# Performance work log

Hardware: AMD Instinct MI355X
Metric: run time of the kernel (lower is better)

The kernel has to match this reference:

```python
import jax, jax.numpy as jnp
import numpy as np

B, D, H = 512, 1024, 2048          # batch, context_dim, l_hidden
MAX_STEPS = 8                       # config.max_l_steps
ATOL = 0.01                         # config.l_conv_atol
THR = 0.1                           # config.commitment_threshold


def setup_inputs() -> dict:
    key = jax.random.key(0)
    ks = jax.random.split(key, 20)
    mat = lambda k, shp, fi: jax.random.normal(k, shp, jnp.float32) / np.float32(np.sqrt(fi))
    inp = dict(
        enc=jax.random.normal(ks[0], (B, D), jnp.float32),
        static_context=jax.random.normal(ks[1], (B, D), jnp.float32),
        # fresh RWKV state: channel 3 (pp, running max-exponent) = -1e30
        l_state=jnp.zeros((B, H, 5), jnp.float32).at[:, :, 3].set(-1e30),
        initial_drift=0.1 * jax.random.normal(ks[2], (B, D), jnp.float32),
        # l_input_proj: Linear(2*D -> H)
        Win=mat(ks[3], (2 * D, H), 2 * D), b_in=jnp.zeros((H,), jnp.float32),
        # context_drift_proj: Linear(H -> D, bias=False)
        Wdrift=mat(ks[4], (H, D), H),
        # l_to_out: Linear(H -> D)
        Wout=mat(ks[5], (H, D), H), b_out=jnp.zeros((D,), jnp.float32),
        # RWKV cell (v4-style) parameters over hidden dim H
        mix_k=jax.random.uniform(ks[6], (H,), jnp.float32),
        mix_v=jax.random.uniform(ks[7], (H,), jnp.float32),
        mix_r=jax.random.uniform(ks[8], (H,), jnp.float32),
        mix_k2=jax.random.uniform(ks[9], (H,), jnp.float32),
        mix_r2=jax.random.uniform(ks[10], (H,), jnp.float32),
        time_decay=0.5 * jax.random.normal(ks[11], (H,), jnp.float32),
        time_first=0.5 * jax.random.normal(ks[12], (H,), jnp.float32),
        Wk=mat(ks[13], (H, H), H), Wv=mat(ks[14], (H, H), H),
        Wr=mat(ks[15], (H, H), H), Wo=mat(ks[16], (H, H), H),
        Wk2=mat(ks[17], (H, H), H), Wv2=mat(ks[18], (H, H), H),
        Wr2=mat(ks[19], (H, H), H),
    )
    return inp


def _forward(enc, static_context, l_state, initial_drift, Win, b_in, Wdrift, Wout, b_out,
             mix_k, mix_v, mix_r, mix_k2, mix_r2, time_decay, time_first,
             Wk, Wv, Wr, Wo, Wk2, Wv2, Wr2):
    def cell(x, state):
        # RWKV-style linear-attention cell. state: [B,H,5] = (x_prev_tm, aa, bb, pp, x_prev_cm)
        xx, aa, bb, pp, cc = (state[..., i] for i in range(5))
        xk = x * mix_k + xx * (1.0 - mix_k)
        xv = x * mix_v + xx * (1.0 - mix_v)
        xr = x * mix_r + xx * (1.0 - mix_r)
        r = jax.nn.sigmoid(xr @ Wr)
        k = xk @ Wk
        v = xv @ Wv
        ww = time_first + k
        q = jnp.maximum(pp, ww)
        e1 = jnp.exp(pp - q); e2 = jnp.exp(ww - q)
        wkv = (e1 * aa + e2 * v) / (e1 * bb + e2)
        ww2 = pp - jnp.exp(time_decay)
        q2 = jnp.maximum(ww2, k)
        e1b = jnp.exp(ww2 - q2); e2b = jnp.exp(k - q2)
        tm_out = (r * wkv) @ Wo
        # channel-mix half of the cell (state channel 4)
        xk2 = x * mix_k2 + cc * (1.0 - mix_k2)
        xr2 = x * mix_r2 + cc * (1.0 - mix_r2)
        r2 = jax.nn.sigmoid(xr2 @ Wr2)
        kk = jnp.square(jax.nn.relu(xk2 @ Wk2))
        out = tm_out + r2 * (kk @ Wv2)
        new_state = jnp.stack([x, e1b * aa + e2b * v, e1b * bb + e2b, q2, x], axis=-1)
        return out, new_state

    def l_input_of(drift):
        v = jnp.concatenate([enc, static_context + drift], axis=-1) @ Win + b_in
        return jnp.clip(v, -50.0, 50.0)

    def step(carry, _):
        drift, sstate, done, csum, cnt = carry
        li = l_input_of(drift)
        out, ns = cell(li, sstate)
        ns = jnp.clip(ns, -50.0, 50.0)
        delta = jnp.tanh(out @ Wdrift)
        nd = jnp.clip(drift + delta, -5.0, 5.0)
        hinge = jnp.minimum(jax.nn.relu(jnp.mean(jnp.sum(nd * nd, axis=-1)) - THR), 100.0)
        conv = jnp.mean(jnp.abs(delta)) < ATOL
        # freeze all updates once converged (early-exit semantics under jit)
        drift = jnp.where(done, drift, nd)
        sstate = jnp.where(done, sstate, ns)
        csum = jnp.where(done, csum, csum + hinge)
        cnt = jnp.where(done, cnt, cnt + 1.0)
        done = jnp.logical_or(done, conv)
        return (drift, sstate, done, csum, cnt), None

    carry0 = (initial_drift, l_state, jnp.array(False), jnp.float32(0.0), jnp.float32(0.0))
    (drift, _, _, csum, cnt), _ = jax.lax.scan(step, carry0, None, length=MAX_STEPS)

    # final commit step uses the ORIGINAL l_state (not the shadow state)
    li = l_input_of(drift)
    final_out, next_state = cell(li, l_state)
    next_state = jnp.clip(next_state, -50.0, 50.0)
    final_enc = enc + final_out @ Wout + b_out
    commitment = csum / jnp.maximum(cnt, 1.0)
    return final_enc, next_state, commitment, drift


def reference(enc, static_context, l_state, initial_drift, Win, b_in, Wdrift, Wout, b_out,
              mix_k, mix_v, mix_r, mix_k2, mix_r2, time_decay, time_first,
              Wk, Wv, Wr, Wo, Wk2, Wv2, Wr2):
    return _forward(enc, static_context, l_state, initial_drift, Win, b_in, Wdrift, Wout, b_out,
                    mix_k, mix_v, mix_r, mix_k2, mix_r2, time_decay, time_first,
                    Wk, Wv, Wr, Wo, Wk2, Wv2, Wr2)
```

## Files before the change

### kernel.cpp

```cpp
#include <hip/hip_runtime.h>
#include <hip/hip_bf16.h>

#define Bb 512
#define Dd 1024
#define Hh 2048
#define BH_ (Bb*Hh)
#define BD_ (Bb*Dd)

typedef unsigned short u16;
typedef __attribute__((ext_vector_type(8))) short short8;
typedef __attribute__((ext_vector_type(4))) float f32x4;

enum { M_F32 = 0, M_IN, M_SIG, M_SQRELU, M_MIX, M_BF16, M_DRIFT, M_FINAL };

struct GemmP {
    const u16* A[5];
    const u16* W[5];
    void* dst[5];
    int mode[5];
    int M, N, K;
    int dstride;
    const int* done;
    const float* bias;
    const float* mk; const float* mv; const float* mr; const float* mk2v; const float* mr2v;
    float* xx; float* cc;
    const float* lstate;
    float* liF;
    float* stateOut;
    u16 *o1, *o2, *o3, *o4, *o5;
    const float* Kp; const float* Vp; const float* Rp;
    float* aa; float* bbp; float* ppp;
    const float* Li;
    const float* tf; const float* td;
    const float* R2;
    u16* acat35;
    float* drift; float* accAbs; float* accSq;
    float* scal; int nticket;
    const float* enc; const float* bout; float* dout;
    const float* sc; u16* acat;
};

#define GLDS16(gp, lp) __builtin_amdgcn_global_load_lds( \
    (const __attribute__((address_space(1))) void*)(gp), \
    (__attribute__((address_space(3))) void*)(lp), 16, 0, 0)

template <int NB>
__global__ __launch_bounds__(512, 2) void gemm_T(GemmP p) {
    if (p.done && *(volatile const int*)p.done) return;
    const int z = blockIdx.z;
    const u16* __restrict__ A = p.A[z];
    const u16* __restrict__ W = p.W[z];
    const int Kd = p.K;

    const int nbx = gridDim.x;
    const int P = nbx >> 3;
    const int local = (int)blockIdx.y * nbx + (int)blockIdx.x;
    const int cxcd = local & 7, j = local >> 3;
    const int bx = cxcd * P + (j % P);
    const int by = j / P;
    const int m0 = by * 64, n0 = bx * 64;

    __shared__ alignas(16) u16 smem[2 * NB][64 * 64];

    const int t = threadIdx.x;
    const int l = t & 63, w = t >> 6;
    const int lane16 = l & 15, quad = l >> 4;
    const int wq = w & 3, kg = w >> 2;
    const int wm = wq & 1, wn = wq >> 1;

    const int srow = t >> 3, sc8 = t & 7;
    const int scs = sc8 ^ (srow & 7);
    const u16* ag = A + (size_t)(m0 + srow) * Kd + scs * 8;
    const u16* bg = W + (size_t)(n0 + srow) * Kd + scs * 8;

    f32x4 zero = {0.f, 0.f, 0.f, 0.f};
    f32x4 acc[2][2];
    acc[0][0] = zero; acc[0][1] = zero; acc[1][0] = zero; acc[1][1] = zero;

    const int nslab = Kd >> 6;
#pragma unroll
    for (int i = 0; i < NB - 1; ++i) {
        GLDS16(ag + (size_t)i * 64, &smem[i][512 * w]);
        GLDS16(bg + (size_t)i * 64, &smem[NB + i][512 * w]);
    }

    int bcur = 0;
    for (int t2 = 0; t2 < nslab; ++t2) {
        int ahead = nslab - 1 - t2; if (ahead > NB - 2) ahead = NB - 2;
        switch (ahead) {
            case 4:  asm volatile("s_waitcnt vmcnt(8)" ::: "memory"); break;
            case 3:  asm volatile("s_waitcnt vmcnt(6)" ::: "memory"); break;
            case 2:  asm volatile("s_waitcnt vmcnt(4)" ::: "memory"); break;
            case 1:  asm volatile("s_waitcnt vmcnt(2)" ::: "memory"); break;
            default: asm volatile("s_waitcnt vmcnt(0)" ::: "memory"); break;
        }
        __builtin_amdgcn_sched_barrier(0);
        __builtin_amdgcn_s_barrier();
        __builtin_amdgcn_sched_barrier(0);

        const u16* As = smem[bcur];
        const u16* Bs = smem[NB + bcur];
        const int cg = kg * 4 + quad;
        const int ra0 = wm * 32 + lane16, ra1 = ra0 + 16;
        const int rb0 = wn * 32 + lane16, rb1 = rb0 + 16;
        short8 af0 = *(const short8*)(const void*)&As[ra0 * 64 + ((cg ^ (ra0 & 7)) << 3)];
        short8 af1 = *(const short8*)(const void*)&As[ra1 * 64 + ((cg ^ (ra1 & 7)) << 3)];
        short8 bf0 = *(const short8*)(const void*)&Bs[rb0 * 64 + ((cg ^ (rb0 & 7)) << 3)];
        short8 bf1 = *(const short8*)(const void*)&Bs[rb1 * 64 + ((cg ^ (rb1 & 7)) << 3)];

        if (t2 + NB - 1 < nslab) {
            const int bst = (bcur == 0) ? NB - 1 : bcur - 1;
            GLDS16(ag + (size_t)(t2 + NB - 1) * 64, &smem[bst][512 * w]);
            GLDS16(bg + (size_t)(t2 + NB - 1) * 64, &smem[NB + bst][512 * w]);
        }

        acc[0][0] = __builtin_amdgcn_mfma_f32_16x16x32_bf16(af0, bf0, acc[0][0], 0, 0, 0);
        acc[0][1] = __builtin_amdgcn_mfma_f32_16x16x32_bf16(af0, bf1, acc[0][1], 0, 0, 0);
        acc[1][0] = __builtin_amdgcn_mfma_f32_16x16x32_bf16(af1, bf0, acc[1][0], 0, 0, 0);
        acc[1][1] = __builtin_amdgcn_mfma_f32_16x16x32_bf16(af1, bf1, acc[1][1], 0, 0, 0);
        __builtin_amdgcn_sched_barrier(0);
        bcur = (bcur + 1 == NB) ? 0 : bcur + 1;
    }
    __syncthreads();

    float* red = (float*)smem;
    const int rbase = wq * 1088 + l * 17;
    if (kg == 1) {
#pragma unroll
        for (int sm = 0; sm < 2; ++sm)
#pragma unroll
            for (int sn = 0; sn < 2; ++sn)
#pragma unroll
                for (int i = 0; i < 4; ++i)
                    red[rbase + (sm * 2 + sn) * 4 + i] = acc[sm][sn][i];
    }
    __syncthreads();

    const int mode = p.mode[z];
    float sabs = 0.f, ssq = 0.f;
    if (kg == 0) {
#pragma unroll
        for (int sm = 0; sm < 2; ++sm)
#pragma unroll
            for (int sn = 0; sn < 2; ++sn)
#pragma unroll
                for (int i = 0; i < 4; ++i) {
                    const int m = m0 + wm * 32 + sm * 16 + quad * 4 + i;
                    const int n = n0 + wn * 32 + sn * 16 + lane16;
                    const size_t idx = (size_t)m * p.N + n;
                    const float v = acc[sm][sn][i] + red[rbase + (sm * 2 + sn) * 4 + i];
                    if (mode == M_F32) {
                        ((float*)p.dst[z])[idx] = v;
                    } else if (mode == M_IN) {
                        float li = fminf(fmaxf(v + p.bias[n], -50.f), 50.f);
                        float xxv, ccv;
                        if (p.lstate) { xxv = p.lstate[idx * 5 + 0]; ccv = p.lstate[idx * 5 + 4]; }
                        else { xxv = p.xx[idx]; ccv = p.cc[idx]; }
                        float mk = p.mk[n], mv = p.mv[n], mr = p.mr[n], mk2 = p.mk2v[n], mr2 = p.mr2v[n];
                        ((__hip_bfloat16*)p.o1)[idx] = __float2bfloat16(li * mk + xxv * (1.f - mk));
                        ((__hip_bfloat16*)p.o2)[idx] = __float2bfloat16(li * mv + xxv * (1.f - mv));
                        ((__hip_bfloat16*)p.o3)[idx] = __float2bfloat16(li * mr + xxv * (1.f - mr));
                        ((__hip_bfloat16*)p.o4)[idx] = __float2bfloat16(li * mk2 + ccv * (1.f - mk2));
                        ((__hip_bfloat16*)p.o5)[idx] = __float2bfloat16(li * mr2 + ccv * (1.f - mr2));
                        if (p.lstate) { p.stateOut[idx * 5 + 0] = li; p.stateOut[idx * 5 + 4] = li; }
                        else p.liF[idx] = li;
                    } else if (mode == M_SIG) {
                        ((float*)p.dst[z])[idx] = 1.f / (1.f + __expf(-v));
                    } else if (mode == M_SQRELU) {
                        float r = fmaxf(v, 0.f);
                        ((__hip_bfloat16*)p.dst[z])[idx] = __float2bfloat16(r * r);
                    } else if (mode == M_BF16) {
                        ((__hip_bfloat16*)p.dst[z])[(size_t)m * p.dstride + n] = __float2bfloat16(v);
                    } else if (mode == M_MIX) {
                        float k = p.Kp[idx], vv = p.Vp[idx], rpre = p.Rp[idx];
                        float a, b, P5;
                        if (p.lstate) { a = p.lstate[idx * 5 + 1]; b = p.lstate[idx * 5 + 2]; P5 = p.lstate[idx * 5 + 3]; }
                        else { a = p.aa[idx]; b = p.bbp[idx]; P5 = p.ppp[idx]; }
                        float r = 1.f / (1.f + __expf(-rpre));
                        float ww = p.tf[n] + k;
                        float q = fmaxf(P5, ww);
                        float e1 = __expf(P5 - q), e2 = __expf(ww - q);
                        float wkv = (e1 * a + e2 * vv) / (e1 * b + e2);
                        const size_t i35 = (size_t)m * 4096 + n;
                        ((__hip_bfloat16*)p.acat35)[i35] = __float2bfloat16(r * wkv);
                        ((__hip_bfloat16*)p.acat35)[i35 + 2048] = __float2bfloat16(p.R2[idx] * v);
                        float ww2 = P5 - __expf(p.td[n]);
                        float q2 = fmaxf(ww2, k);
                        float e1b = __expf(ww2 - q2), e2b = __expf(k - q2);
                        float na  = fminf(fmaxf(e1b * a + e2b * vv, -50.f), 50.f);
                        float nb2 = fminf(fmaxf(e1b * b + e2b, -50.f), 50.f);
                        float nq  = fminf(fmaxf(q2, -50.f), 50.f);
                        if (p.lstate) {
                            p.stateOut[idx * 5 + 1] = na; p.stateOut[idx * 5 + 2] = nb2; p.stateOut[idx * 5 + 3] = nq;
                        } else {
                            p.aa[idx] = na; p.bbp[idx] = nb2; p.ppp[idx] = nq;
                            float li = p.Li[idx];
                            p.xx[idx] = li; p.cc[idx] = li;
                        }
                    } else if (mode == M_DRIFT) {
                        float d = tanhf(v);
                        float nd = fminf(fmaxf(p.drift[idx] + d, -5.f), 5.f);
                        p.drift[idx] = nd;
                        ((__hip_bfloat16*)p.acat)[(size_t)m * 2048 + 1024 + n] = __float2bfloat16(p.sc[idx] + nd);
                        sabs += fabsf(d);
                        ssq += nd * nd;
                    } else {
                        p.dout[idx] = p.enc[idx] + v + p.bout[n];
                    }
                }
    }

    if (mode == M_DRIFT) {
        if (kg == 0) {
#pragma unroll
            for (int off = 32; off > 0; off >>= 1) {
                sabs += __shfl_down(sabs, off, 64);
                ssq += __shfl_down(ssq, off, 64);
            }
            if (l == 0) { atomicAdd(p.accAbs, sabs); atomicAdd(p.accSq, ssq); }
        }
        __syncthreads();
        if (t == 0) {
            __threadfence();
            int vtk = atomicAdd((int*)(p.scal + 5), 1);
            if (vtk == p.nticket - 1) {
                volatile float* s = p.scal;
                float hinge = fminf(fmaxf(s[4] / (float)Bb - 0.1f, 0.f), 100.f);
                s[1] = s[1] + hinge;
                s[2] = s[2] + 1.f;
                if (s[3] / (float)BD_ < 0.01f) ((volatile int*)p.scal)[0] = 1;
                s[3] = 0.f; s[4] = 0.f;
                ((volatile int*)p.scal)[5] = 0;
            }
        }
    }
}

struct TP { const float* src[7]; u16* dst[7]; int K; int N; };

__global__ void transposeWz(TP tp) {
    __shared__ float tile[32][33];
    const float* __restrict__ src = tp.src[blockIdx.z];
    u16* __restrict__ dst = tp.dst[blockIdx.z];
    int kt = blockIdx.y * 32, nt = blockIdx.x * 32;
    int tx = threadIdx.x, ty = threadIdx.y;
#pragma unroll
    for (int j = 0; j < 4; j++)
        tile[ty + j * 8][tx] = src[(size_t)(kt + ty + j * 8) * tp.N + nt + tx];
    __syncthreads();
    __hip_bfloat16* d = (__hip_bfloat16*)dst;
#pragma unroll
    for (int j = 0; j < 4; j++)
        d[(size_t)(nt + ty + j * 8) * tp.K + kt + tx] = __float2bfloat16(tile[tx][ty + j * 8]);
}

__global__ void castW(const float* __restrict__ src, u16* __restrict__ dst, int nelem) {
    int i = blockIdx.x * 256 + threadIdx.x;
    if (i < nelem) ((__hip_bfloat16*)dst)[i] = __float2bfloat16(src[i]);
}

struct CP { const u16* src[2]; u16* dst[2]; };
__global__ void copyTail(CP cp) {
    int i = blockIdx.x * 256 + threadIdx.x;
    if (i >= Dd * Hh) return;
    const u16* s = cp.src[blockIdx.z];
    u16* d = cp.dst[blockIdx.z];
    int m = i >> 11, k = i & 2047;
    d[(size_t)m * 4096 + 2048 + k] = s[i];
}

__global__ void initstate(const float* __restrict__ lstate, const float* __restrict__ idrift,
                          const float* __restrict__ enc, const float* __restrict__ sc,
                          float* xx, float* aa, float* bb, float* pp, float* cc,
                          float* drift, float* scal, u16* acat) {
    int i = blockIdx.x * 256 + threadIdx.x;
    if (i < BH_) {
        const float* s = lstate + (size_t)i * 5;
        xx[i] = s[0]; aa[i] = s[1]; bb[i] = s[2]; pp[i] = s[3]; cc[i] = s[4];
    }
    if (i < BD_) {
        drift[i] = idrift[i];
        int m = i >> 10, d = i & 1023;
        __hip_bfloat16* Ab = (__hip_bfloat16*)acat;
        Ab[(size_t)m * 2048 + d] = __float2bfloat16(enc[i]);
        Ab[(size_t)m * 2048 + 1024 + d] = __float2bfloat16(sc[i] + idrift[i]);
    }
    if (i == 0) {
        ((int*)scal)[0] = 0; scal[1] = 0.f; scal[2] = 0.f; scal[3] = 0.f; scal[4] = 0.f;
        ((int*)scal)[5] = 0;
    }
}

__global__ void tailk(const float* __restrict__ scal, const float* __restrict__ drift, float* __restrict__ dout) {
    int i = blockIdx.x * 256 + threadIdx.x;
    const size_t OC = (size_t)BD_ + (size_t)5 * BH_;
    if (i == 0) dout[OC] = scal[1] / fmaxf(scal[2], 1.f);
    if (i < BD_) dout[OC + 1 + i] = drift[i];
}

extern "C" void kernel_launch(void* const* d_in, const int* in_sizes, int n_in,
                              void* d_out, int out_size, void* d_ws, size_t ws_size,
                              hipStream_t stream) {
    const float* enc    = (const float*)d_in[0];
    const float* sc     = (const float*)d_in[1];
    const float* lstate = (const float*)d_in[2];
    const float* idrift = (const float*)d_in[3];
    const float* Win    = (const float*)d_in[4];
    const float* b_in   = (const float*)d_in[5];
    const float* Wdrift = (const float*)d_in[6];
    const float* Wout   = (const float*)d_in[7];
    const float* b_out  = (const float*)d_in[8];
    const float* mix_k  = (const float*)d_in[9];
    const float* mix_v  = (const float*)d_in[10];
    const float* mix_r  = (const float*)d_in[11];
    const float* mix_k2 = (const float*)d_in[12];
    const float* mix_r2 = (const float*)d_in[13];
    const float* tdec   = (const float*)d_in[14];
    const float* tfirst = (const float*)d_in[15];
    const float* Wk  = (const float*)d_in[16];
    const float* Wv  = (const float*)d_in[17];
    const float* Wr  = (const float*)d_in[18];
    const float* Wo  = (const float*)d_in[19];
    const float* Wk2 = (const float*)d_in[20];
    const float* Wv2 = (const float*)d_in[21];
    const float* Wr2 = (const float*)d_in[22];
    float* dout = (float*)d_out;

    const size_t BHs = (size_t)Bb * Hh;
    const size_t BDs = (size_t)Bb * Dd;

    const size_t need_f32 = 10 * BHs + BDs + 16;
    const size_t need_u16 = (size_t)2 * Dd * Hh + 6 * (size_t)Hh * Hh + 2 * (size_t)Hh * Dd
                          + 2 * (size_t)Dd * 4096 + 7 * BHs + (size_t)Bb * 4096;
    const size_t need_bytes = need_f32 * 4 + need_u16 * 2;
    if (ws_size < need_bytes) return;

    float* f = (float*)d_ws;
    float* xx  = f;
    float* aa  = xx + BHs;
    float* bbp = aa + BHs;
    float* ppp = bbp + BHs;
    float* cc  = ppp + BHs;
    float* Li  = cc + BHs;
    float* Kp  = Li + BHs;
    float* Vp  = Kp + BHs;
    float* Rp  = Vp + BHs;
    float* R2  = Rp + BHs;
    float* drift = R2 + BHs;
    float* scal  = drift + BDs;
    u16* u = (u16*)(scal + 16);
    u16* WinT  = u; u += (size_t)2 * Dd * Hh;
    u16* WkT   = u; u += (size_t)Hh * Hh;
    u16* WvT   = u; u += (size_t)Hh * Hh;
    u16* WrT   = u; u += (size_t)Hh * Hh;
    u16* Wk2T  = u; u += (size_t)Hh * Hh;
    u16* Wv2T  = u; u += (size_t)Hh * Hh;
    u16* Wr2T  = u; u += (size_t)Hh * Hh;
    u16* WdT   = u; u += (size_t)Hh * Dd;
    u16* WoutT = u; u += (size_t)Hh * Dd;
    u16* W35   = u; u += (size_t)Dd * 4096;
    u16* W35F  = u; u += (size_t)Dd * 4096;
    u16* Acat  = u; u += BHs;
    u16* Xk    = u; u += BHs;
    u16* Xv    = u; u += BHs;
    u16* Xr    = u; u += BHs;
    u16* Xk2   = u; u += BHs;
    u16* Xr2   = u; u += BHs;
    u16* Kk    = u; u += BHs;
    u16* Acat35 = u; u += (size_t)Bb * 4096;
    u16* Wo_bf = Xk;

    int* doneptr = (int*)scal;
    float* accAbs = scal + 3;
    float* accSq  = scal + 4;

    dim3 tb(32, 8);
    TP tpa = {};
    tpa.src[0] = Wk;  tpa.dst[0] = WkT;
    tpa.src[1] = Wv;  tpa.dst[1] = WvT;
    tpa.src[2] = Wr;  tpa.dst[2] = WrT;
    tpa.src[3] = Wk2; tpa.dst[3] = Wk2T;
    tpa.src[4] = Wv2; tpa.dst[4] = Wv2T;
    tpa.src[5] = Wr2; tpa.dst[5] = Wr2T;
    tpa.K = Hh; tpa.N = Hh;
    transposeWz<<<dim3(Hh / 32, Hh / 32, 6), tb, 0, stream>>>(tpa);
    TP tpb = {};
    tpb.src[0] = Win; tpb.dst[0] = WinT; tpb.K = 2 * Dd; tpb.N = Hh;
    transposeWz<<<dim3(Hh / 32, (2 * Dd) / 32, 1), tb, 0, stream>>>(tpb);
    TP tpc = {};
    tpc.src[0] = Wdrift; tpc.dst[0] = WdT;
    tpc.src[1] = Wout;   tpc.dst[1] = WoutT;
    tpc.K = Hh; tpc.N = Dd;
    transposeWz<<<dim3(Dd / 32, Hh / 32, 2), tb, 0, stream>>>(tpc);

    castW<<<(Hh * Hh + 255) / 256, 256, 0, stream>>>(Wo, Wo_bf, Hh * Hh);

    initstate<<<(BH_ + 255) / 256, 256, 0, stream>>>(lstate, idrift, enc, sc,
                                                     xx, aa, bbp, ppp, cc, drift, scal, Acat);

    GemmP pp = {};
    pp.A[0] = WdT;   pp.W[0] = Wo_bf; pp.mode[0] = M_BF16; pp.dst[0] = W35;
    pp.A[1] = WoutT; pp.W[1] = Wo_bf; pp.mode[1] = M_BF16; pp.dst[1] = W35F;
    pp.M = Dd; pp.N = Hh; pp.K = Hh; pp.dstride = 4096;
    gemm_T<3><<<dim3(Hh / 64, Dd / 64, 2), 512, 0, stream>>>(pp);

    CP cpt = {};
    cpt.src[0] = WdT;   cpt.dst[0] = W35;
    cpt.src[1] = WoutT; cpt.dst[1] = W35F;
    copyTail<<<dim3((Dd * Hh + 255) / 256, 1, 2), 256, 0, stream>>>(cpt);

    GemmP g1 = {};
    g1.A[0] = Acat; g1.W[0] = WinT; g1.mode[0] = M_IN;
    g1.M = Bb; g1.N = Hh; g1.K = 2 * Dd;
    g1.done = doneptr;
    g1.bias = b_in; g1.mk = mix_k; g1.mv = mix_v; g1.mr = mix_r; g1.mk2v = mix_k2; g1.mr2v = mix_r2;
    g1.xx = xx; g1.cc = cc; g1.liF = Li;
    g1.o1 = Xk; g1.o2 = Xv; g1.o3 = Xr; g1.o4 = Xk2; g1.o5 = Xr2;

    GemmP g2 = {};
    g2.A[0] = Xk;  g2.W[0] = WkT;  g2.mode[0] = M_F32;    g2.dst[0] = Kp;
    g2.A[1] = Xv;  g2.W[1] = WvT;  g2.mode[1] = M_F32;    g2.dst[1] = Vp;
    g2.A[2] = Xr;  g2.W[2] = WrT;  g2.mode[2] = M_F32;    g2.dst[2] = Rp;
    g2.A[3] = Xr2; g2.W[3] = Wr2T; g2.mode[3] = M_SIG;    g2.dst[3] = R2;
    g2.A[4] = Xk2; g2.W[4] = Wk2T; g2.mode[4] = M_SQRELU; g2.dst[4] = Kk;
    g2.M = Bb; g2.N = Hh; g2.K = Hh;
    g2.done = doneptr;

    GemmP g2b = {};
    g2b.A[0] = Kk; g2b.W[0] = Wv2T; g2b.mode[0] = M_MIX;
    g2b.M = Bb; g2b.N = Hh; g2b.K = Hh;
    g2b.done = doneptr;
    g2b.Kp = Kp; g2b.Vp = Vp; g2b.Rp = Rp;
    g2b.aa = aa; g2b.bbp = bbp; g2b.ppp = ppp;
    g2b.xx = xx; g2b.cc = cc; g2b.Li = Li;
    g2b.tf = tfirst; g2b.td = tdec;
    g2b.R2 = R2; g2b.acat35 = Acat35;

    GemmP g35 = {};
    g35.A[0] = Acat35; g35.W[0] = W35; g35.mode[0] = M_DRIFT;
    g35.M = Bb; g35.N = Dd; g35.K = 4096;
    g35.done = doneptr;
    g35.drift = drift; g35.accAbs = accAbs; g35.accSq = accSq;
    g35.scal = scal; g35.nticket = (Dd / 64) * (Bb / 64);
    g35.sc = sc; g35.acat = Acat;

    dim3 gH(Hh / 64, Bb / 64, 1);
    dim3 gH5(Hh / 64, Bb / 64, 5);
    dim3 gD(Dd / 64, Bb / 64, 1);

    for (int s = 0; s < 8; ++s) {
        gemm_T<6><<<gH,  512, 0, stream>>>(g1);
        gemm_T<3><<<gH5, 512, 0, stream>>>(g2);
        gemm_T<6><<<gH,  512, 0, stream>>>(g2b);
        gemm_T<6><<<gD,  512, 0, stream>>>(g35);
    }

    float* stateOut = dout + BD_;

    GemmP f1p = g1;
    f1p.done = nullptr; f1p.lstate = lstate; f1p.stateOut = stateOut;
    gemm_T<6><<<gH, 512, 0, stream>>>(f1p);

    GemmP f2p = g2; f2p.done = nullptr;
    gemm_T<3><<<gH5, 512, 0, stream>>>(f2p);

    GemmP f2bp = g2b;
    f2bp.done = nullptr; f2bp.lstate = lstate; f2bp.stateOut = stateOut;
    gemm_T<6><<<gH, 512, 0, stream>>>(f2bp);

    GemmP f35p = {};
    f35p.A[0] = Acat35; f35p.W[0] = W35F; f35p.mode[0] = M_FINAL;
    f35p.M = Bb; f35p.N = Dd; f35p.K = 4096;
    f35p.enc = enc; f35p.bout = b_out; f35p.dout = dout;
    gemm_T<6><<<gD, 512, 0, stream>>>(f35p);

    tailk<<<(BD_ + 255) / 256, 256, 0, stream>>>(scal, drift, dout);
}
```

Measured before the change: 1.658 ms.

## Add 32-row-tile GEMM kernel with 128-wide K slabs for single-GEMM launches

Introduces a new gemm_s kernel that uses 32x64 output tiles with 128-wide K slabs and a 3-stage LDS ring, and uses it for the input, mix and drift/final GEMMs. Halving the M tile doubles the block count for these small-N grids so more CUs are occupied, and the wider K slab cuts the number of barrier iterations. The shared epilogue and drift reduction are factored into helper functions, and the drift ticket count is updated to match the new grid. The gemm_T waitcnt cases for 4, 3 and 2 slabs ahead are removed, so those fall through to vmcnt(0) in the NB=3 template that is still used. The trade-off is more redundant loading of B tiles across the extra blocks.

```diff
diff --git a/kernel.cpp b/kernel.cpp
--- a/kernel.cpp
+++ b/kernel.cpp
@@ -44,6 +44,94 @@
     (const __attribute__((address_space(1))) void*)(gp), \
     (__attribute__((address_space(3))) void*)(lp), 16, 0, 0)
 
+__device__ __forceinline__ void epilog(const GemmP& p, int z, int mode, int m, int n, float v,
+                                       float& sabs, float& ssq) {
+    const size_t idx = (size_t)m * p.N + n;
+    if (mode == M_F32) {
+        ((float*)p.dst[z])[idx] = v;
+    } else if (mode == M_IN) {
+        float li = fminf(fmaxf(v + p.bias[n], -50.f), 50.f);
+        float xxv, ccv;
+        if (p.lstate) { xxv = p.lstate[idx * 5 + 0]; ccv = p.lstate[idx * 5 + 4]; }
+        else { xxv = p.xx[idx]; ccv = p.cc[idx]; }
+        float mk = p.mk[n], mv = p.mv[n], mr = p.mr[n], mk2 = p.mk2v[n], mr2 = p.mr2v[n];
+        ((__hip_bfloat16*)p.o1)[idx] = __float2bfloat16(li * mk + xxv * (1.f - mk));
+        ((__hip_bfloat16*)p.o2)[idx] = __float2bfloat16(li * mv + xxv * (1.f - mv));
+        ((__hip_bfloat16*)p.o3)[idx] = __float2bfloat16(li * mr + xxv * (1.f - mr));
+        ((__hip_bfloat16*)p.o4)[idx] = __float2bfloat16(li * mk2 + ccv * (1.f - mk2));
+        ((__hip_bfloat16*)p.o5)[idx] = __float2bfloat16(li * mr2 + ccv * (1.f - mr2));
+        if (p.lstate) { p.stateOut[idx * 5 + 0] = li; p.stateOut[idx * 5 + 4] = li; }
+        else p.liF[idx] = li;
+    } else if (mode == M_SIG) {
+        ((float*)p.dst[z])[idx] = 1.f / (1.f + __expf(-v));
+    } else if (mode == M_SQRELU) {
+        float r = fmaxf(v, 0.f);
+        ((__hip_bfloat16*)p.dst[z])[idx] = __float2bfloat16(r * r);
+    } else if (mode == M_BF16) {
+        ((__hip_bfloat16*)p.dst[z])[(size_t)m * p.dstride + n] = __float2bfloat16(v);
+    } else if (mode == M_MIX) {
+        float k = p.Kp[idx], vv = p.Vp[idx], rpre = p.Rp[idx];
+        float a, b, P5;
+        if (p.lstate) { a = p.lstate[idx * 5 + 1]; b = p.lstate[idx * 5 + 2]; P5 = p.lstate[idx * 5 + 3]; }
+        else { a = p.aa[idx]; b = p.bbp[idx]; P5 = p.ppp[idx]; }
+        float r = 1.f / (1.f + __expf(-rpre));
+        float ww = p.tf[n] + k;
+        float q = fmaxf(P5, ww);
+        float e1 = __expf(P5 - q), e2 = __expf(ww - q);
+        float wkv = (e1 * a + e2 * vv) / (e1 * b + e2);
+        const size_t i35 = (size_t)m * 4096 + n;
+        ((__hip_bfloat16*)p.acat35)[i35] = __float2bfloat16(r * wkv);
+        ((__hip_bfloat16*)p.acat35)[i35 + 2048] = __float2bfloat16(p.R2[idx] * v);
+        float ww2 = P5 - __expf(p.td[n]);
+        float q2 = fmaxf(ww2, k);
+        float e1b = __expf(ww2 - q2), e2b = __expf(k - q2);
+        float na  = fminf(fmaxf(e1b * a + e2b * vv, -50.f), 50.f);
+        float nb2 = fminf(fmaxf(e1b * b + e2b, -50.f), 50.f);
+        float nq  = fminf(fmaxf(q2, -50.f), 50.f);
+        if (p.lstate) {
+            p.stateOut[idx * 5 + 1] = na; p.stateOut[idx * 5 + 2] = nb2; p.stateOut[idx * 5 + 3] = nq;
+        } else {
+            p.aa[idx] = na; p.bbp[idx] = nb2; p.ppp[idx] = nq;
+            float li = p.Li[idx];
+            p.xx[idx] = li; p.cc[idx] = li;
+        }
+    } else if (mode == M_DRIFT) {
+        float d = tanhf(v);
+        float nd = fminf(fmaxf(p.drift[idx] + d, -5.f), 5.f);
+        p.drift[idx] = nd;
+        ((__hip_bfloat16*)p.acat)[(size_t)m * 2048 + 1024 + n] = __float2bfloat16(p.sc[idx] + nd);
+        sabs += fabsf(d);
+        ssq += nd * nd;
+    } else {
+        p.dout[idx] = p.enc[idx] + v + p.bout[n];
+    }
+}
+
+__device__ __forceinline__ void driftTail(const GemmP& p, int t, int l, int kg, float sabs, float ssq) {
+    if (kg == 0) {
+#pragma unroll
+        for (int off = 32; off > 0; off >>= 1) {
+            sabs += __shfl_down(sabs, off, 64);
+            ssq += __shfl_down(ssq, off, 64);
+        }
+        if (l == 0) { atomicAdd(p.accAbs, sabs); atomicAdd(p.accSq, ssq); }
+    }
+    __syncthreads();
+    if (t == 0) {
+        __threadfence();
+        int vtk = atomicAdd((int*)(p.scal + 5), 1);
+        if (vtk == p.nticket - 1) {
+            volatile float* s = p.scal;
+            float hinge = fminf(fmaxf(s[4] / (float)Bb - 0.1f, 0.f), 100.f);
+            s[1] = s[1] + hinge;
+            s[2] = s[2] + 1.f;
+            if (s[3] / (float)BD_ < 0.01f) ((volatile int*)p.scal)[0] = 1;
+            s[3] = 0.f; s[4] = 0.f;
+            ((volatile int*)p.scal)[5] = 0;
+        }
+    }
+}
+
 template <int NB>
 __global__ __launch_bounds__(512, 2) void gemm_T(GemmP p) {
     if (p.done && *(volatile const int*)p.done) return;
@@ -88,9 +176,6 @@
     for (int t2 = 0; t2 < nslab; ++t2) {
         int ahead = nslab - 1 - t2; if (ahead > NB - 2) ahead = NB - 2;
         switch (ahead) {
-            case 4:  asm volatile("s_waitcnt vmcnt(8)" ::: "memory"); break;
-            case 3:  asm volatile("s_waitcnt vmcnt(6)" ::: "memory"); break;
-            case 2:  asm volatile("s_waitcnt vmcnt(4)" ::: "memory"); break;
             case 1:  asm volatile("s_waitcnt vmcnt(2)" ::: "memory"); break;
             default: asm volatile("s_waitcnt vmcnt(0)" ::: "memory"); break;
         }
@@ -147,93 +232,117 @@
                 for (int i = 0; i < 4; ++i) {
                     const int m = m0 + wm * 32 + sm * 16 + quad * 4 + i;
                     const int n = n0 + wn * 32 + sn * 16 + lane16;
-                    const size_t idx = (size_t)m * p.N + n;
                     const float v = acc[sm][sn][i] + red[rbase + (sm * 2 + sn) * 4 + i];
-                    if (mode == M_F32) {
-                        ((float*)p.dst[z])[idx] = v;
-                    } else if (mode == M_IN) {
-                        float li = fminf(fmaxf(v + p.bias[n], -50.f), 50.f);
-                        float xxv, ccv;
-                        if (p.lstate) { xxv = p.lstate[idx * 5 + 0]; ccv = p.lstate[idx * 5 + 4]; }
-                        else { xxv = p.xx[idx]; ccv = p.cc[idx]; }
-                        float mk = p.mk[n], mv = p.mv[n], mr = p.mr[n], mk2 = p.mk2v[n], mr2 = p.mr2v[n];
-                        ((__hip_bfloat16*)p.o1)[idx] = __float2bfloat16(li * mk + xxv * (1.f - mk));
-                        ((__hip_bfloat16*)p.o2)[idx] = __float2bfloat16(li * mv + xxv * (1.f - mv));
-                        ((__hip_bfloat16*)p.o3)[idx] = __float2bfloat16(li * mr + xxv * (1.f - mr));
-                        ((__hip_bfloat16*)p.o4)[idx] = __float2bfloat16(li * mk2 + ccv * (1.f - mk2));
-                        ((__hip_bfloat16*)p.o5)[idx] = __float2bfloat16(li * mr2 + ccv * (1.f - mr2));
-                        if (p.lstate) { p.stateOut[idx * 5 + 0] = li; p.stateOut[idx * 5 + 4] = li; }
-                        else p.liF[idx] = li;
-                    } else if (mode == M_SIG) {
-                        ((float*)p.dst[z])[idx] = 1.f / (1.f + __expf(-v));
-                    } else if (mode == M_SQRELU) {
-                        float r = fmaxf(v, 0.f);
-                        ((__hip_bfloat16*)p.dst[z])[idx] = __float2bfloat16(r * r);
-                    } else if (mode == M_BF16) {
-                        ((__hip_bfloat16*)p.dst[z])[(size_t)m * p.dstride + n] = __float2bfloat16(v);
-                    } else if (mode == M_MIX) {
-                        float k = p.Kp[idx], vv = p.Vp[idx], rpre = p.Rp[idx];
-                        float a, b, P5;
-                        if (p.lstate) { a = p.lstate[idx * 5 + 1]; b = p.lstate[idx * 5 + 2]; P5 = p.lstate[idx * 5 + 3]; }
-                        else { a = p.aa[idx]; b = p.bbp[idx]; P5 = p.ppp[idx]; }
-                        float r = 1.f / (1.f + __expf(-rpre));
-                        float ww = p.tf[n] + k;
-                        float q = fmaxf(P5, ww);
-                        float e1 = __expf(P5 - q), e2 = __expf(ww - q);
-                        float wkv = (e1 * a + e2 * vv) / (e1 * b + e2);
-                        const size_t i35 = (size_t)m * 4096 + n;
-                        ((__hip_bfloat16*)p.acat35)[i35] = __float2bfloat16(r * wkv);
-                        ((__hip_bfloat16*)p.acat35)[i35 + 2048] = __float2bfloat16(p.R2[idx] * v);
-                        float ww2 = P5 - __expf(p.td[n]);
-                        float q2 = fmaxf(ww2, k);
-                        float e1b = __expf(ww2 - q2), e2b = __expf(k - q2);
-                        float na  = fminf(fmaxf(e1b * a + e2b * vv, -50.f), 50.f);
-                        float nb2 = fminf(fmaxf(e1b * b + e2b, -50.f), 50.f);
-                        float nq  = fminf(fmaxf(q2, -50.f), 50.f);
-                        if (p.lstate) {
-                            p.stateOut[idx * 5 + 1] = na; p.stateOut[idx * 5 + 2] = nb2; p.stateOut[idx * 5 + 3] = nq;
-                        } else {
-                            p.aa[idx] = na; p.bbp[idx] = nb2; p.ppp[idx] = nq;
-                            float li = p.Li[idx];
-                            p.xx[idx] = li; p.cc[idx] = li;
-                        }
-                    } else if (mode == M_DRIFT) {
-                        float d = tanhf(v);
-                        float nd = fminf(fmaxf(p.drift[idx] + d, -5.f), 5.f);
-                        p.drift[idx] = nd;
-                        ((__hip_bfloat16*)p.acat)[(size_t)m * 2048 + 1024 + n] = __float2bfloat16(p.sc[idx] + nd);
-                        sabs += fabsf(d);
-                        ssq += nd * nd;
-                    } else {
-                        p.dout[idx] = p.enc[idx] + v + p.bout[n];
-                    }
+                    epilog(p, z, mode, m, n, v, sabs, ssq);
                 }
     }
-
-    if (mode == M_DRIFT) {
-        if (kg == 0) {
-#pragma unroll
-            for (int off = 32; off > 0; off >>= 1) {
-                sabs += __shfl_down(sabs, off, 64);
-                ssq += __shfl_down(ssq, off, 64);
+    if (mode == M_DRIFT) driftTail(p, t, l, kg, sabs, ssq);
+}
+
+__global__ __launch_bounds__(512, 2) void gemm_s(GemmP p) {
+    if (p.done && *(volatile const int*)p.done) return;
+    const int z = blockIdx.z;
+    const u16* __restrict__ A = p.A[z];
+    const u16* __restrict__ W = p.W[z];
+    const int Kd = p.K;
+
+    const int nbx = gridDim.x;
+    const int P = nbx >> 3;
+    const int local = (int)blockIdx.y * nbx + (int)blockIdx.x;
+    const int cxcd = local & 7, j = local >> 3;
+    const int bx = cxcd * P + (j % P);
+    const int by = j / P;
+    const int m0 = by * 32, n0 = bx * 64;
+
+    __shared__ alignas(16) u16 sA[3][4096];
+    __shared__ alignas(16) u16 sB[3][8192];
+
+    const int t = threadIdx.x;
+    const int l = t & 63, w = t >> 6;
+    const int lane16 = l & 15, quad = l >> 4;
+    const int wq = w & 3, kg = w >> 2;
+    const int wm = wq & 1, wn = wq >> 1;
+
+    const int arow = t >> 4, c16 = t & 15;
+    const int csrc = c16 ^ (arow & 15);
+    const u16* ag  = A + (size_t)(m0 + arow) * Kd + csrc * 8;
+    const u16* bg1 = W + (size_t)(n0 + arow) * Kd + csrc * 8;
+    const u16* bg2 = W + (size_t)(n0 + 32 + arow) * Kd + csrc * 8;
+
+    f32x4 zero = {0.f, 0.f, 0.f, 0.f};
+    f32x4 acc[2];
+    acc[0] = zero; acc[1] = zero;
+
+    const int nslab = Kd >> 7;
+#pragma unroll
+    for (int i = 0; i < 2; ++i) {
+        GLDS16(ag  + (size_t)i * 128, &sA[i][512 * w]);
+        GLDS16(bg1 + (size_t)i * 128, &sB[i][512 * w]);
+        GLDS16(bg2 + (size_t)i * 128, &sB[i][4096 + 512 * w]);
+    }
+
+    int bcur = 0;
+    for (int t2 = 0; t2 < nslab; ++t2) {
+        if (t2 < nslab - 1) asm volatile("s_waitcnt vmcnt(3)" ::: "memory");
+        else                asm volatile("s_waitcnt vmcnt(0)" ::: "memory");
+        __builtin_amdgcn_sched_barrier(0);
+        __builtin_amdgcn_s_barrier();
+        __builtin_amdgcn_sched_barrier(0);
+
+        const u16* As = sA[bcur];
+        const u16* Bs = sB[bcur];
+        const int ra  = wm * 16 + lane16;
+        const int rb0 = wn * 32 + lane16, rb1 = rb0 + 16;
+        const int cg0 = kg * 8 + quad;
+        const int cg1 = cg0 + 4;
+        short8 a0  = *(const short8*)(const void*)&As[ra  * 128 + ((cg0 ^ (ra  & 15)) << 3)];
+        short8 a1  = *(const short8*)(const void*)&As[ra  * 128 + ((cg1 ^ (ra  & 15)) << 3)];
+        short8 b00 = *(const short8*)(const void*)&Bs[rb0 * 128 + ((cg0 ^ (rb0 & 15)) << 3)];
+        short8 b10 = *(const short8*)(const void*)&Bs[rb1 * 128 + ((cg0 ^ (rb1 & 15)) << 3)];
+        short8 b01 = *(const short8*)(const void*)&Bs[rb0 * 128 + ((cg1 ^ (rb0 & 15)) << 3)];
+        short8 b11 = *(const short8*)(const void*)&Bs[rb1 * 128 + ((cg1 ^ (rb1 & 15)) << 3)];
+
+        if (t2 + 2 < nslab) {
+            const int bst = (bcur == 0) ? 2 : bcur - 1;
+            GLDS16(ag  + (size_t)(t2 + 2) * 128, &sA[bst][512 * w]);
+            GLDS16(bg1 + (size_t)(t2 + 2) * 128, &sB[bst][512 * w]);
+            GLDS16(bg2 + (size_t)(t2 + 2) * 128, &sB[bst][4096 + 512 * w]);
+        }
+
+        acc[0] = __builtin_amdgcn_mfma_f32_16x16x32_bf16(a0, b00, acc[0], 0, 0, 0);
+        acc[1] = __builtin_amdgcn_mfma_f32_16x16x32_bf16(a0, b10, acc[1], 0, 0, 0);
+        acc[0] = __builtin_amdgcn_mfma_f32_16x16x32_bf16(a1, b01, acc[0], 0, 0, 0);
+        acc[1] = __builtin_amdgcn_mfma_f32_16x16x32_bf16(a1, b11, acc[1], 0, 0, 0);
+        __builtin_amdgcn_sched_barrier(0);
+        bcur = (bcur + 1 == 3) ? 0 : bcur + 1;
+    }
+    __syncthreads();
+
+    float* red = (float*)sA;
+    const int rbase = wq * 576 + l * 9;
+    if (kg == 1) {
+#pragma unroll
+        for (int nf = 0; nf < 2; ++nf)
+#pragma unroll
+            for (int i = 0; i < 4; ++i)
+                red[rbase + nf * 4 + i] = acc[nf][i];
+    }
+    __syncthreads();
+
+    const int mode = p.mode[z];
+    float sabs = 0.f, ssq = 0.f;
+    if (kg == 0) {
+#pragma unroll
+        for (int nf = 0; nf < 2; ++nf)
+#pragma unroll
+            for (int i = 0; i < 4; ++i) {
+                const int m = m0 + wm * 16 + quad * 4 + i;
+                const int n = n0 + wn * 32 + nf * 16 + lane16;
+                const float v = acc[nf][i] + red[rbase + nf * 4 + i];
+                epilog(p, z, mode, m, n, v, sabs, ssq);
             }
-            if (l == 0) { atomicAdd(p.accAbs, sabs); atomicAdd(p.accSq, ssq); }
-        }
-        __syncthreads();
-        if (t == 0) {
-            __threadfence();
-            int vtk = atomicAdd((int*)(p.scal + 5), 1);
-            if (vtk == p.nticket - 1) {
-                volatile float* s = p.scal;
-                float hinge = fminf(fmaxf(s[4] / (float)Bb - 0.1f, 0.f), 100.f);
-                s[1] = s[1] + hinge;
-                s[2] = s[2] + 1.f;
-                if (s[3] / (float)BD_ < 0.01f) ((volatile int*)p.scal)[0] = 1;
-                s[3] = 0.f; s[4] = 0.f;
-                ((volatile int*)p.scal)[5] = 0;
-            }
-        }
-    }
+    }
+    if (mode == M_DRIFT) driftTail(p, t, l, kg, sabs, ssq);
 }
 
 struct TP { const float* src[7]; u16* dst[7]; int K; int N; };
@@ -441,38 +550,38 @@
     g35.M = Bb; g35.N = Dd; g35.K = 4096;
     g35.done = doneptr;
     g35.drift = drift; g35.accAbs = accAbs; g35.accSq = accSq;
-    g35.scal = scal; g35.nticket = (Dd / 64) * (Bb / 64);
+    g35.scal = scal; g35.nticket = (Dd / 64) * (Bb / 32);
     g35.sc = sc; g35.acat = Acat;
 
-    dim3 gH(Hh / 64, Bb / 64, 1);
     dim3 gH5(Hh / 64, Bb / 64, 5);
-    dim3 gD(Dd / 64, Bb / 64, 1);
+    dim3 gS(Hh / 64, Bb / 32, 1);
+    dim3 gSD(Dd / 64, Bb / 32, 1);
 
     for (int s = 0; s < 8; ++s) {
-        gemm_T<6><<<gH,  512, 0, stream>>>(g1);
+        gemm_s<<<gS,  512, 0, stream>>>(g1);
         gemm_T<3><<<gH5, 512, 0, stream>>>(g2);
-        gemm_T<6><<<gH,  512, 0, stream>>>(g2b);
-        gemm_T<6><<<gD,  512, 0, stream>>>(g35);
+        gemm_s<<<gS,  512, 0, stream>>>(g2b);
+        gemm_s<<<gSD, 512, 0, stream>>>(g35);
     }
 
     float* stateOut = dout + BD_;
 
     GemmP f1p = g1;
     f1p.done = nullptr; f1p.lstate = lstate; f1p.stateOut = stateOut;
-    gemm_T<6><<<gH, 512, 0, stream>>>(f1p);
+    gemm_s<<<gS, 512, 0, stream>>>(f1p);
 
     GemmP f2p = g2; f2p.done = nullptr;
     gemm_T<3><<<gH5, 512, 0, stream>>>(f2p);
 
     GemmP f2bp = g2b;
     f2bp.done = nullptr; f2bp.lstate = lstate; f2bp.stateOut = stateOut;
-    gemm_T<6><<<gH, 512, 0, stream>>>(f2bp);
+    gemm_s<<<gS, 512, 0, stream>>>(f2bp);
 
     GemmP f35p = {};
     f35p.A[0] = Acat35; f35p.W[0] = W35F; f35p.mode[0] = M_FINAL;
     f35p.M = Bb; f35p.N = Dd; f35p.K = 4096;
     f35p.enc = enc; f35p.bout = b_out; f35p.dout = dout;
-    gemm_T<6><<<gD, 512, 0, stream>>>(f35p);
+    gemm_s<<<gSD, 512, 0, stream>>>(f35p);
 
     tailk<<<(BD_ + 255) / 256, 256, 0, stream>>>(scal, drift, dout);
 }
```

Result: no change. 1.633 ms (-1.5%).
